# Optimization experiments

Hardware: AMD Instinct MI355X
Metric: run time of the kernel (lower is better)

Reference implementation:

```python
import jax, jax.numpy as jnp
import numpy as np

N, E, C, F = 20000, 320000, 64, 8
DIN = 2 * C + F + 1           # MLP input: sender scalars + receiver scalars + radial feats + length
AVG = 16.0                    # avg_num_neighbors
INV_SQRT3 = 0.5773502691896258


def setup_inputs() -> dict:
    key = jax.random.key(0)
    ks = jax.random.split(key, 16)
    d = {}
    d["node_feats"] = jax.random.normal(ks[0], (N, C + 3 * C), jnp.float32)  # 64x0e + 64x1o (mul-major)
    d["edge_attrs"] = jax.random.normal(ks[1], (E, 4), jnp.float32)           # SH: 1x0e + 1x1o
    d["edge_feats"] = jax.random.normal(ks[2], (E, F), jnp.float32)           # radial basis
    d["lengths"] = jax.random.uniform(ks[3], (E, 1), jnp.float32)
    d["edge_index"] = jax.random.randint(ks[4], (2, E), 0, N, jnp.int32)      # (sender, receiver)
    d["Wsc"] = jax.random.normal(ks[5], (C, C), jnp.float32) / np.sqrt(C).astype(np.float32)
    d["Wup0"] = jax.random.normal(ks[6], (C, C), jnp.float32) / np.sqrt(C).astype(np.float32)
    d["Wup1"] = jax.random.normal(ks[7], (C, C), jnp.float32) / np.sqrt(C).astype(np.float32)
    d["W1"] = jax.random.normal(ks[8], (DIN, C), jnp.float32) / np.sqrt(DIN).astype(np.float32)
    d["b1"] = jnp.zeros((C,), jnp.float32)
    d["W2"] = jax.random.normal(ks[9], (C, C), jnp.float32) / np.sqrt(C).astype(np.float32)
    d["b2"] = jnp.zeros((C,), jnp.float32)
    d["W3"] = jax.random.normal(ks[10], (C, 4 * C), jnp.float32) * 1e-3       # near-zero init like the source
    d["Ws"] = jax.random.normal(ks[11], (2 * C, C), jnp.float32) / np.sqrt(2 * C).astype(np.float32)
    d["Wv"] = jax.random.normal(ks[12], (2 * C, C), jnp.float32) / np.sqrt(2 * C).astype(np.float32)
    return d


def reference(node_feats, edge_attrs, edge_feats, lengths, edge_index,
              Wsc, Wup0, Wup1, W1, b1, W2, b2, W3, Ws, Wv):
    n = node_feats.shape[0]
    s = node_feats[:, :C]                          # [N,C] scalar (0e) channels
    v = node_feats[:, C:].reshape(n, C, 3)         # [N,C,3] vector (1o) channels

    node_scalars = s @ Wsc                          # linear_scalar -> 64x0e
    s_up = s @ Wup0                                 # linear_up, 0e block
    v_up = jnp.einsum('nci,cd->ndi', v, Wup1)       # linear_up, 1o block

    snd, rcv = edge_index[0], edge_index[1]

    # weight MLP: Dense->silu->Dense->silu->Dense(no bias)
    mlp_in = jnp.concatenate([node_scalars[snd], node_scalars[rcv], edge_feats, lengths], axis=-1)
    h = jax.nn.silu(mlp_in @ W1 + b1)
    h = jax.nn.silu(h @ W2 + b2)
    tw = h @ W3                                     # [E, 4C] per-irrep tp weights
    w0, w1, w2, w3 = jnp.split(tw, 4, axis=-1)

    y0 = edge_attrs[:, :1]                          # [E,1] SH l=0
    y1 = edge_attrs[:, 1:4]                         # [E,3] SH l=1
    xs = s_up[snd]                                  # [E,C]   gather senders
    xv = v_up[snd]                                  # [E,C,3]

    # weighted tensor product paths (component normalization), filtered to 0e/1o
    p0 = xs * y0 * w0                                               # 0e x 0e -> 0e  [E,C]
    p1 = (jnp.einsum('eci,ei->ec', xv, y1) * INV_SQRT3) * w1        # 1o x 1o -> 0e  [E,C]
    p2 = xs[:, :, None] * y1[:, None, :] * w2[:, :, None]           # 0e x 1o -> 1o  [E,C,3]
    p3 = xv * y0[:, :, None] * w3[:, :, None]                       # 1o x 0e -> 1o  [E,C,3]

    # scatter_sum messages into receiver nodes
    m0 = jax.ops.segment_sum(jnp.concatenate([p0, p1], axis=-1), rcv, num_segments=n)  # [N,2C]
    m1 = jax.ops.segment_sum(jnp.concatenate([p2, p3], axis=1), rcv, num_segments=n)   # [N,2C,3]

    # final equivariant linear on simplified irreps_mid (128x0e + 128x1o), / avg_num_neighbors
    out_s = (m0 @ Ws) / AVG                          # [N,C]
    out_v = jnp.einsum('nci,cd->ndi', m1, Wv) / AVG  # [N,C,3]

    # reshape_irreps -> [N, channels, 1 + 3]
    return jnp.concatenate([out_s[:, :, None], out_v], axis=-1)
```

## Files before the change

### kernel.cpp

```cpp
#include <hip/hip_runtime.h>

#define N_NODES 20000
#define N_EDGES 320000
#define INV_SQRT3 0.5773502691896258f

typedef unsigned short u16;
typedef unsigned int u32;
typedef __attribute__((ext_vector_type(8))) short short8;
typedef __attribute__((ext_vector_type(8))) _Float16 half8;
typedef __attribute__((ext_vector_type(2))) __fp16 fp16x2;
typedef __attribute__((ext_vector_type(4))) float f32x4;
typedef __attribute__((ext_vector_type(4))) u32 u32x4v;

static const size_t OFF_NSBF = 0;
static const size_t OFF_SV   = 2560000;
static const size_t OFF_MG   = 23040000;
static const size_t OFF_TW   = 64000000;
static const size_t OFF_W1F  = 227840000;
static const size_t OFF_W2F  = 227860480;
static const size_t OFF_W3F  = 227868672;
static const size_t OFF_WNF  = 227901440;
static const size_t OFF_CNT  = 227950592;
static const size_t OFF_OFFS = 228030592;
static const size_t OFF_CUR  = 228110608;
static const size_t OFF_SS   = 229470608;
static const size_t OFF_RS   = 230750608;
static const size_t OFF_EA   = 232030608;
static const size_t OFF_EF   = 237150608;
static const size_t OFF_LEN  = 242270608;

static __device__ __forceinline__ u16 f2bf(float x) {
    union { float f; u32 u; } c; c.f = x;
    u32 u = c.u + 0x7fffu + ((c.u >> 16) & 1u);
    return (u16)(u >> 16);
}
static __device__ __forceinline__ float bf2f(u16 b) {
    union { u32 u; float f; } c; c.u = (u32)b << 16; return c.f;
}
static __device__ __forceinline__ u16 f2h(float x) {
    union { _Float16 h; u16 u; } c; c.h = (_Float16)x; return c.u;
}
static __device__ __forceinline__ float h2f(u32 b) {
    union { u16 u; _Float16 h; } c; c.u = (u16)b; return (float)c.h;
}
static __device__ __forceinline__ u32 pkh(float a, float b) {
    union { fp16x2 h; u32 u; } c;
    c.h = __builtin_amdgcn_cvt_pkrtz(a, b);
    return c.u;
}
static __device__ __forceinline__ f32x4 mfma16(short8 a, short8 b, f32x4 c) {
    return __builtin_amdgcn_mfma_f32_16x16x32_bf16(a, b, c, 0, 0, 0);
}
static __device__ __forceinline__ f32x4 mfma16h(half8 a, half8 b, f32x4 c) {
    return __builtin_amdgcn_mfma_f32_16x16x32_f16(a, b, c, 0, 0, 0);
}
static __device__ __forceinline__ float silu(float x) {
    return x / (1.0f + __expf(-x));
}
template <typename T>
static __device__ __forceinline__ T ntload(const T* p) { return __builtin_nontemporal_load(p); }
template <typename T>
static __device__ __forceinline__ void ntstore(T* p, T v) { __builtin_nontemporal_store(v, p); }

__global__ void prep_w_kernel(const float* __restrict__ W1, const float* __restrict__ W2,
                              const float* __restrict__ W3,
                              u16* __restrict__ W1f, u16* __restrict__ W2f, u16* __restrict__ W3f) {
    int t = blockIdx.x * 256 + threadIdx.x;
    if (t >= 3840) return;
    int l = t & 63, grp = t >> 6;
    int hi = l >> 4, lo = l & 15;
    if (grp < 20) {
        int kk = grp >> 2, jt = grp & 3;
#pragma unroll
        for (int e2 = 0; e2 < 8; e2++) {
            int k = kk * 32 + hi * 8 + e2, j = jt * 16 + lo;
            W1f[(size_t)(grp * 64 + l) * 8 + e2] = (k < 137) ? f2bf(W1[k * 64 + j]) : (u16)0;
        }
    } else if (grp < 28) {
        int g = grp - 20; int kk = g >> 2, jt = g & 3;
#pragma unroll
        for (int e2 = 0; e2 < 8; e2++) {
            int k = kk * 32 + hi * 8 + e2, j = jt * 16 + lo;
            int kp = ((k & 3) << 4) + (k >> 2);
            W2f[(size_t)(g * 64 + l) * 8 + e2] = f2h(W2[kp * 64 + j]);
        }
    } else {
        int g = grp - 28; int kk = g >> 4, jt = g & 15;
#pragma unroll
        for (int e2 = 0; e2 < 8; e2++) {
            int k = kk * 32 + hi * 8 + e2, j = jt * 16 + lo;
            int kp = ((k & 3) << 4) + (k >> 2);
            W3f[(size_t)(g * 64 + l) * 8 + e2] = f2h(W3[kp * 256 + j]);
        }
    }
}

__global__ void prep_wn_kernel(const float* __restrict__ Wsc, const float* __restrict__ Wup0,
                               const float* __restrict__ Wup1, u16* __restrict__ WNF) {
    int t = blockIdx.x * 256 + threadIdx.x;
    if (t >= 1536) return;
    int mat = t >> 9;
    int rem = t & 511;
    int g = rem >> 6, l = rem & 63;
    int kk = g >> 2, jt = g & 3, hi = l >> 4, lo = l & 15;
    const float* W = (mat == 0) ? Wsc : (mat == 1) ? Wup0 : Wup1;
    u16* dh = WNF + (size_t)mat * 8192 + (size_t)(g * 64 + l) * 8;
    u16* dl = dh + 4096;
#pragma unroll
    for (int e2 = 0; e2 < 8; e2++) {
        int k = kk * 32 + hi * 8 + e2, d = jt * 16 + lo;
        float w = W[k * 64 + d];
        u16 h = f2bf(w);
        dh[e2] = h;
        dl[e2] = f2bf(w - bf2f(h));
    }
}

__global__ void prep_w2_kernel(const float* __restrict__ Ws, const float* __restrict__ Wv,
                               u16* __restrict__ WSF) {
    int t = blockIdx.x * 256 + threadIdx.x;
    if (t >= 2048) return;
    int l = t & 63, grp = t >> 6;
    int wsel = grp >> 4;
    int g = grp & 15;
    int kk = g >> 2, jt = g & 3;
    int hi = l >> 4, lo = l & 15;
    const float* W = wsel ? Wv : Ws;
    u16* dh = WSF + (size_t)wsel * 16384;
    u16* dl = dh + 8192;
    size_t base = (size_t)(g * 64 + l) * 8;
#pragma unroll
    for (int e2 = 0; e2 < 8; e2++) {
        int k = kk * 32 + hi * 8 + e2, d = jt * 16 + lo;
        float w = W[k * 64 + d];
        u16 h = f2bf(w);
        float r = w - bf2f(h);
        dh[base + e2] = h;
        dl[base + e2] = f2bf(r);
    }
}

__global__ __launch_bounds__(256) void node_prep_kernel(
    const float* __restrict__ node_feats, const u16* __restrict__ WNF,
    u16* __restrict__ ns_bf, u16* __restrict__ svh) {
    const int tid = threadIdx.x;
    const int lane = tid & 63;
    const int w = tid >> 6;
    const int lo16 = lane & 15;
    const int hi = lane >> 4;
    const int nb = blockIdx.x * 64 + w * 16;

    int an = nb + lo16; if (an > N_NODES - 1) an = N_NODES - 1;
    const float* arow = node_feats + (size_t)an * 256;

    const short8* B = (const short8*)WNF;

    f32x4 acc_ns[4], acc_su[4], acc_v[3][4];
#pragma unroll
    for (int jt = 0; jt < 4; jt++) {
        acc_ns[jt] = (f32x4)(0.0f);
        acc_su[jt] = (f32x4)(0.0f);
#pragma unroll
        for (int i = 0; i < 3; i++) acc_v[i][jt] = (f32x4)(0.0f);
    }

#pragma unroll
    for (int kk = 0; kk < 2; kk++) {
        short8 sh, sl;
        {
            const float* sp = arow + kk * 32 + hi * 8;
            f32x4 x0 = *(const f32x4*)sp;
            f32x4 x1 = *(const f32x4*)(sp + 4);
#pragma unroll
            for (int j = 0; j < 4; j++) {
                u16 h0 = f2bf(x0[j]);
                sh[j] = (short)h0;
                sl[j] = (short)f2bf(x0[j] - bf2f(h0));
                u16 h1 = f2bf(x1[j]);
                sh[4 + j] = (short)h1;
                sl[4 + j] = (short)f2bf(x1[j] - bf2f(h1));
            }
        }
        short8 vh[3], vl[3];
#pragma unroll
        for (int i = 0; i < 3; i++) {
            const float* vp = arow + 64 + i + 3 * (kk * 32 + hi * 8);
#pragma unroll
            for (int e = 0; e < 8; e++) {
                float x = vp[e * 3];
                u16 hb = f2bf(x);
                vh[i][e] = (short)hb;
                vl[i][e] = (short)f2bf(x - bf2f(hb));
            }
        }
#pragma unroll
        for (int jt = 0; jt < 4; jt++) {
            int fi = (kk * 4 + jt) * 64 + lane;
            short8 bh = B[fi], bl = B[512 + fi];
            acc_ns[jt] = mfma16(sh, bh, acc_ns[jt]);
            acc_ns[jt] = mfma16(sl, bh, acc_ns[jt]);
            acc_ns[jt] = mfma16(sh, bl, acc_ns[jt]);
            bh = B[1024 + fi]; bl = B[1536 + fi];
            acc_su[jt] = mfma16(sh, bh, acc_su[jt]);
            acc_su[jt] = mfma16(sl, bh, acc_su[jt]);
            acc_su[jt] = mfma16(sh, bl, acc_su[jt]);
            bh = B[2048 + fi]; bl = B[2560 + fi];
#pragma unroll
            for (int i = 0; i < 3; i++) {
                acc_v[i][jt] = mfma16(vh[i], bh, acc_v[i][jt]);
                acc_v[i][jt] = mfma16(vl[i], bh, acc_v[i][jt]);
                acc_v[i][jt] = mfma16(vh[i], bl, acc_v[i][jt]);
            }
        }
    }

#pragma unroll
    for (int r = 0; r < 4; r++) {
        int n = nb + hi * 4 + r;
        if (n < N_NODES) {
#pragma unroll
            for (int jt = 0; jt < 4; jt++) {
                int d = jt * 16 + lo16;
                ns_bf[(size_t)n * 64 + d] = f2bf(acc_ns[jt][r]);
                uint2 o;
                o.x = pkh(acc_su[jt][r], acc_v[0][jt][r]);
                o.y = pkh(acc_v[1][jt][r], acc_v[2][jt][r]);
                *(uint2*)&svh[((size_t)n * 64 + d) * 4] = o;
            }
        }
    }
}

__global__ void hist_kernel(const int* __restrict__ ei, int* __restrict__ cnt) {
    int e = blockIdx.x * 256 + threadIdx.x;
    if (e < N_EDGES) atomicAdd(&cnt[ei[N_EDGES + e]], 1);
}

__global__ void scan_kernel(const int* __restrict__ cnt, int* __restrict__ offs,
                            int* __restrict__ cursor) {
    __shared__ int buf[1024];
    int t = threadIdx.x;
    int base = t * 20;
    int loc[20];
    int tot = 0;
    int v20[20];
    if (base < N_NODES) {
#pragma unroll
        for (int q = 0; q < 5; q++) {
            int4 vv = *(const int4*)&cnt[base + q * 4];
            v20[q * 4 + 0] = vv.x; v20[q * 4 + 1] = vv.y;
            v20[q * 4 + 2] = vv.z; v20[q * 4 + 3] = vv.w;
        }
    } else {
#pragma unroll
        for (int i = 0; i < 20; i++) v20[i] = 0;
    }
#pragma unroll
    for (int i = 0; i < 20; i++) { loc[i] = tot; tot += v20[i]; }
    buf[t] = tot;
    __syncthreads();
    for (int d = 1; d < 1024; d <<= 1) {
        int add = (t >= d) ? buf[t - d] : 0;
        __syncthreads();
        buf[t] += add;
        __syncthreads();
    }
    int ebase = buf[t] - tot;
#pragma unroll
    for (int i = 0; i < 20; i++) {
        int idx = base + i;
        if (idx < N_NODES) { int o = ebase + loc[i]; offs[idx] = o; cursor[idx] = o; }
    }
    if (t == 1023) offs[N_NODES] = buf[1023];
}

__global__ void scatter_kernel(const int* __restrict__ ei, const float* __restrict__ edge_attrs,
                               const float* __restrict__ edge_feats, const float* __restrict__ lengths,
                               int* __restrict__ cursor,
                               int* __restrict__ ssort, int* __restrict__ rsort,
                               float* __restrict__ easort, u16* __restrict__ efsort,
                               u16* __restrict__ lsort) {
    int e = blockIdx.x * 256 + threadIdx.x;
    if (e < N_EDGES) {
        int sn = ei[e];
        int rc = ei[N_EDGES + e];
        float4 ea = *(const float4*)(edge_attrs + (size_t)e * 4);
        float4 f0 = *(const float4*)(edge_feats + (size_t)e * 8);
        float4 f1 = *(const float4*)(edge_feats + (size_t)e * 8 + 4);
        float len = lengths[e];
        uint4 pk;
        pk.x = (u32)f2bf(f0.x) | ((u32)f2bf(f0.y) << 16);
        pk.y = (u32)f2bf(f0.z) | ((u32)f2bf(f0.w) << 16);
        pk.z = (u32)f2bf(f1.x) | ((u32)f2bf(f1.y) << 16);
        pk.w = (u32)f2bf(f1.z) | ((u32)f2bf(f1.w) << 16);
        int pos = atomicAdd(&cursor[rc], 1);
        ssort[pos] = sn;
        rsort[pos] = rc;
        *(float4*)(easort + (size_t)pos * 4) = ea;
        *(uint4*)(efsort + (size_t)pos * 8) = pk;
        lsort[pos] = f2bf(len);
    }
}

__global__ __launch_bounds__(256, 5) void mlp_kernel(
    const u16* __restrict__ ns_bf,
    const u16* __restrict__ W1f, const u16* __restrict__ W2f, const u16* __restrict__ W3f,
    const float* __restrict__ b1, const float* __restrict__ b2,
    const int* __restrict__ ssort, const int* __restrict__ rsort,
    const u16* __restrict__ efsort, const u16* __restrict__ lsort,
    u16* __restrict__ twg) {

    __shared__ u16 mlpbuf[64][168];
    __shared__ u16 h1s[64][72];
    u16* h2sf = &mlpbuf[0][0];

    const int tid = threadIdx.x;
    const int l = tid & 63;
    const int lo16 = l & 15;
    const int hi = l >> 4;
    const int w = tid >> 6;
    const int erow = (w << 4) | lo16;
    const int koff = hi * 8;
    const int drow = (w << 4) + hi * 4;

    const int p0 = blockIdx.x * 64;

    const short8* w1frag = (const short8*)W1f;
    const half8* w2frag = (const half8*)W2f;
    const half8* w3frag = (const half8*)W3f;

    float bb1[4], bb2[4];
#pragma unroll
    for (int jt = 0; jt < 4; jt++) { bb1[jt] = b1[jt * 16 + lo16]; bb2[jt] = b2[jt * 16 + lo16]; }

    {
        int rr = tid >> 2, pp = tid & 3;
        uint4 z = {0, 0, 0, 0};
        *(uint4*)&mlpbuf[rr][136 + pp * 8] = z;
    }

    {
        int es = tid >> 2, part = tid & 3;
        int sn = ssort[p0 + es];
        int rc = rsort[p0 + es];
        const uint4* ps = (const uint4*)(ns_bf + (size_t)sn * 64 + part * 16);
        uint4 s0 = ps[0], s1 = ps[1];
        *(uint4*)&mlpbuf[es][part * 16] = s0;
        *(uint4*)&mlpbuf[es][part * 16 + 8] = s1;
        const uint4* pr = (const uint4*)(ns_bf + (size_t)rc * 64 + part * 16);
        uint4 r0v = pr[0], r1v = pr[1];
        *(uint4*)&mlpbuf[es][64 + part * 16] = r0v;
        *(uint4*)&mlpbuf[es][64 + part * 16 + 8] = r1v;
        if (part == 0) {
            uint4 pk = *(const uint4*)(efsort + (size_t)(p0 + es) * 8);
            *(uint4*)&mlpbuf[es][128] = pk;
            mlpbuf[es][136] = lsort[p0 + es];
        }
    }

    f32x4 a1c[4];
#pragma unroll
    for (int jt = 0; jt < 4; jt++) a1c[jt] = (f32x4)(0.0f);
    __builtin_amdgcn_s_setprio(1);
#pragma unroll
    for (int kk = 0; kk < 5; kk++) {
        short8 af = *(const short8*)&mlpbuf[erow][kk * 32 + koff];
        const short8* wb = w1frag + kk * 256 + l;
        a1c[0] = mfma16(af, wb[0],   a1c[0]);
        a1c[1] = mfma16(af, wb[64],  a1c[1]);
        a1c[2] = mfma16(af, wb[128], a1c[2]);
        a1c[3] = mfma16(af, wb[192], a1c[3]);
    }
    __builtin_amdgcn_s_setprio(0);
#pragma unroll
    for (int r = 0; r < 4; r++) {
        uint2 pk;
        pk.x = pkh(silu(a1c[0][r] + bb1[0]), silu(a1c[1][r] + bb1[1]));
        pk.y = pkh(silu(a1c[2][r] + bb1[2]), silu(a1c[3][r] + bb1[3]));
        *(uint2*)&h1s[drow + r][lo16 * 4] = pk;
    }

    f32x4 a2c[4];
#pragma unroll
    for (int jt = 0; jt < 4; jt++) a2c[jt] = (f32x4)(0.0f);
    __builtin_amdgcn_s_setprio(1);
#pragma unroll
    for (int kk = 0; kk < 2; kk++) {
        half8 af = *(const half8*)&h1s[erow][kk * 32 + koff];
        const half8* wb = w2frag + kk * 256 + l;
        a2c[0] = mfma16h(af, wb[0],   a2c[0]);
        a2c[1] = mfma16h(af, wb[64],  a2c[1]);
        a2c[2] = mfma16h(af, wb[128], a2c[2]);
        a2c[3] = mfma16h(af, wb[192], a2c[3]);
    }
    __builtin_amdgcn_s_setprio(0);
#pragma unroll
    for (int r = 0; r < 4; r++) {
        uint2 pk;
        pk.x = pkh(silu(a2c[0][r] + bb2[0]), silu(a2c[1][r] + bb2[1]));
        pk.y = pkh(silu(a2c[2][r] + bb2[2]), silu(a2c[3][r] + bb2[3]));
        *(uint2*)&h2sf[(drow + r) * 72 + lo16 * 4] = pk;
    }

    f32x4 tw[16];
#pragma unroll
    for (int jt = 0; jt < 16; jt++) tw[jt] = (f32x4)(0.0f);
    __builtin_amdgcn_s_setprio(1);
#pragma unroll
    for (int kk = 0; kk < 2; kk++) {
        half8 af = *(const half8*)&h2sf[erow * 72 + kk * 32 + koff];
        const half8* wb = w3frag + kk * 1024 + l;
#pragma unroll
        for (int jt = 0; jt < 16; jt++) tw[jt] = mfma16h(af, wb[jt * 64], tw[jt]);
    }
    __builtin_amdgcn_s_setprio(0);

    int relrow = p0 + drow;
#pragma unroll
    for (int r = 0; r < 4; r++) {
        u16* dst = twg + (size_t)(relrow + r) * 256 + lo16 * 4;
#pragma unroll
        for (int jt4 = 0; jt4 < 4; jt4++) {
            uint2 pk;
            pk.x = pkh(tw[jt4][r],     tw[4 + jt4][r]);
            pk.y = pkh(tw[8 + jt4][r], tw[12 + jt4][r]);
            *(uint2*)(dst + jt4 * 64) = pk;
        }
    }
}

__global__ __launch_bounds__(256, 4) void seg_kernel(
    const u16* __restrict__ svh, const float* __restrict__ easort,
    const int* __restrict__ ssort,
    const int* __restrict__ offs, const u16* __restrict__ twg,
    float* __restrict__ m_g) {
    const int lane = threadIdx.x & 63;
    const int wv = threadIdx.x >> 6;
    const int n = blockIdx.x * 4 + wv;
    const int c = lane;
    const int e0 = offs[n], e1 = offs[n + 1];
    float a_m0 = 0.f, a_m0b = 0.f;
    float a20 = 0.f, a21 = 0.f, a22 = 0.f, a30 = 0.f, a31 = 0.f, a32 = 0.f;
#pragma unroll 4
    for (int pos = e0; pos < e1; ++pos) {
        int sn = ssort[pos];
        uint2 tq = *(const uint2*)(twg + (size_t)pos * 256 + c * 4);
        f32x4 y4 = *(const f32x4*)(easort + (size_t)pos * 4);
        uint2 sp = *(const uint2*)&svh[((size_t)sn * 64 + c) * 4];
        float w0 = h2f(tq.x & 0xffffu);
        float w1 = h2f(tq.x >> 16);
        float w2 = h2f(tq.y & 0xffffu);
        float w3 = h2f(tq.y >> 16);
        float xs  = h2f(sp.x & 0xffffu);
        float xv0 = h2f(sp.x >> 16);
        float xv1 = h2f(sp.y & 0xffffu);
        float xv2 = h2f(sp.y >> 16);
        float y0 = y4.x, ya = y4.y, yb = y4.z, yc = y4.w;
        a_m0 = fmaf(xs * y0, w0, a_m0);
        float dv = xv0 * ya + xv1 * yb + xv2 * yc;
        a_m0b = fmaf(dv, w1, a_m0b);
        float sw2 = xs * w2;
        a20 = fmaf(sw2, ya, a20); a21 = fmaf(sw2, yb, a21); a22 = fmaf(sw2, yc, a22);
        float yw3 = y0 * w3;
        a30 = fmaf(xv0, yw3, a30); a31 = fmaf(xv1, yw3, a31); a32 = fmaf(xv2, yw3, a32);
    }
    float* mr = m_g + (size_t)n * 512;
    ntstore(mr + c,        a_m0);
    ntstore(mr + 64 + c,   a_m0b * INV_SQRT3);
    ntstore(mr + 128 + c,  a20);
    ntstore(mr + 192 + c,  a30);
    ntstore(mr + 256 + c,  a21);
    ntstore(mr + 320 + c,  a31);
    ntstore(mr + 384 + c,  a22);
    ntstore(mr + 448 + c,  a32);
}

__global__ __launch_bounds__(256, 2) void out_kernel(
    const float* __restrict__ m_g, const u16* __restrict__ WSF,
    float* __restrict__ out) {
    const int tid = threadIdx.x;
    const int lane = tid & 63;
    const int w = tid >> 6;
    const int lo16 = lane & 15;
    const int hi = lane >> 4;
    const int nb = blockIdx.x * 64 + w * 16;

    int arow_n = nb + lo16;
    if (arow_n > N_NODES - 1) arow_n = N_NODES - 1;
    const float* arow = m_g + (size_t)arow_n * 512 + hi * 8;

    const short8* bsh = (const short8*)WSF;
    const short8* bsl = (const short8*)(WSF + 8192);
    const short8* bvh = (const short8*)(WSF + 16384);
    const short8* bvl = (const short8*)(WSF + 24576);

    f32x4 acc[4][4];
#pragma unroll
    for (int q = 0; q < 4; q++)
#pragma unroll
        for (int jt = 0; jt < 4; jt++) acc[q][jt] = (f32x4)(0.0f);

#pragma unroll
    for (int kk = 0; kk < 4; kk++) {
        short8 ahi[4], alo[4];
#pragma unroll
        for (int q = 0; q < 4; q++) {
            const float* p = arow + q * 128 + kk * 32;
            f32x4 x0 = ntload((const f32x4*)p);
            f32x4 x1 = ntload((const f32x4*)(p + 4));
#pragma unroll
            for (int j = 0; j < 4; j++) {
                u16 h0 = f2bf(x0[j]);
                ahi[q][j] = (short)h0;
                alo[q][j] = (short)f2bf(x0[j] - bf2f(h0));
                u16 h1 = f2bf(x1[j]);
                ahi[q][4 + j] = (short)h1;
                alo[q][4 + j] = (short)f2bf(x1[j] - bf2f(h1));
            }
        }
#pragma unroll
        for (int jt = 0; jt < 4; jt++) {
            int bidx = (kk * 4 + jt) * 64 + lane;
            short8 wh_s = bsh[bidx];
            short8 wl_s = bsl[bidx];
            short8 wh_v = bvh[bidx];
            short8 wl_v = bvl[bidx];
            acc[0][jt] = mfma16(ahi[0], wh_s, acc[0][jt]);
            acc[0][jt] = mfma16(alo[0], wh_s, acc[0][jt]);
            acc[0][jt] = mfma16(ahi[0], wl_s, acc[0][jt]);
#pragma unroll
            for (int q = 1; q < 4; q++) {
                acc[q][jt] = mfma16(ahi[q], wh_v, acc[q][jt]);
                acc[q][jt] = mfma16(alo[q], wh_v, acc[q][jt]);
                acc[q][jt] = mfma16(ahi[q], wl_v, acc[q][jt]);
            }
        }
    }

#pragma unroll
    for (int r = 0; r < 4; r++) {
        int n = nb + hi * 4 + r;
        if (n < N_NODES) {
#pragma unroll
            for (int jt = 0; jt < 4; jt++) {
                int d = jt * 16 + lo16;
                f32x4 o;
                o.x = acc[0][jt][r] * 0.0625f;
                o.y = acc[1][jt][r] * 0.0625f;
                o.z = acc[2][jt][r] * 0.0625f;
                o.w = acc[3][jt][r] * 0.0625f;
                ntstore((f32x4*)(out + (size_t)n * 256 + d * 4), o);
            }
        }
    }
}

extern "C" void kernel_launch(void* const* d_in, const int* in_sizes, int n_in,
                              void* d_out, int out_size, void* d_ws, size_t ws_size,
                              hipStream_t stream) {
    (void)in_sizes; (void)n_in; (void)out_size; (void)ws_size;
    const float* node_feats = (const float*)d_in[0];
    const float* edge_attrs = (const float*)d_in[1];
    const float* edge_feats = (const float*)d_in[2];
    const float* lengths    = (const float*)d_in[3];
    const int*   edge_index = (const int*)d_in[4];
    const float* Wsc  = (const float*)d_in[5];
    const float* Wup0 = (const float*)d_in[6];
    const float* Wup1 = (const float*)d_in[7];
    const float* W1   = (const float*)d_in[8];
    const float* b1   = (const float*)d_in[9];
    const float* W2   = (const float*)d_in[10];
    const float* b2   = (const float*)d_in[11];
    const float* W3   = (const float*)d_in[12];
    const float* Ws   = (const float*)d_in[13];
    const float* Wv   = (const float*)d_in[14];

    char* ws = (char*)d_ws;
    u16*   ns_bf  = (u16*)(ws + OFF_NSBF);
    u16*   svh    = (u16*)(ws + OFF_SV);
    float* m_g    = (float*)(ws + OFF_MG);
    u16*   twg    = (u16*)(ws + OFF_TW);
    u16*   W1f    = (u16*)(ws + OFF_W1F);
    u16*   W2f    = (u16*)(ws + OFF_W2F);
    u16*   W3f    = (u16*)(ws + OFF_W3F);
    u16*   WNF    = (u16*)(ws + OFF_WNF);
    int*   cnt    = (int*)(ws + OFF_CNT);
    int*   offs   = (int*)(ws + OFF_OFFS);
    int*   cursor = (int*)(ws + OFF_CUR);
    u16*   WSF    = (u16*)(ws + OFF_CUR);
    int*   ssort  = (int*)(ws + OFF_SS);
    int*   rsort  = (int*)(ws + OFF_RS);
    float* easort = (float*)(ws + OFF_EA);
    u16*   efsort = (u16*)(ws + OFF_EF);
    u16*   lsort  = (u16*)(ws + OFF_LEN);
    float* out    = (float*)d_out;

    (void)hipMemsetAsync(cnt, 0, N_NODES * sizeof(int), stream);
    prep_w_kernel<<<15, 256, 0, stream>>>(W1, W2, W3, W1f, W2f, W3f);
    prep_wn_kernel<<<6, 256, 0, stream>>>(Wsc, Wup0, Wup1, WNF);
    node_prep_kernel<<<(N_NODES + 63) / 64, 256, 0, stream>>>(node_feats, WNF, ns_bf, svh);
    hist_kernel<<<N_EDGES / 256, 256, 0, stream>>>(edge_index, cnt);
    scan_kernel<<<1, 1024, 0, stream>>>(cnt, offs, cursor);
    scatter_kernel<<<N_EDGES / 256, 256, 0, stream>>>(edge_index, edge_attrs, edge_feats,
                                                      lengths, cursor,
                                                      ssort, rsort, easort, efsort, lsort);
    prep_w2_kernel<<<8, 256, 0, stream>>>(Ws, Wv, WSF);

    mlp_kernel<<<N_EDGES / 64, 256, 0, stream>>>(ns_bf, W1f, W2f, W3f, b1, b2,
                                                 ssort, rsort, efsort, lsort, twg);
    seg_kernel<<<N_NODES / 4, 256, 0, stream>>>(svh, easort, ssort,
                                                offs, twg, m_g);
    out_kernel<<<(N_NODES + 63) / 64, 256, 0, stream>>>(m_g, WSF, out);
}
```

Baseline: 233.0 us.

## Load MLP input fragments directly from global into registers, skipping LDS staging

The MLP kernel no longer stages sender/receiver scalars and edge features in a 64x168 shared buffer. Each lane now loads its MFMA A-fragments straight from global memory into registers. To make that possible, the scatter kernel writes a padded 32-element per-edge record holding the radial features, the length and zero padding, so the fifth K-chunk is a single aligned load. Shared memory per block drops, and launch bounds go from 5 to 6 blocks per SM for higher occupancy. In exchange, global gather loads are less coalesced (16-byte per-lane reads), the per-edge write in scatter grows to 64 bytes, and register pressure may rise under the tighter launch bound.

```diff
diff --git a/kernel.cpp b/kernel.cpp
--- a/kernel.cpp
+++ b/kernel.cpp
@@ -26,8 +26,7 @@
 static const size_t OFF_SS   = 229470608;
 static const size_t OFF_RS   = 230750608;
 static const size_t OFF_EA   = 232030608;
-static const size_t OFF_EF   = 237150608;
-static const size_t OFF_LEN  = 242270608;
+static const size_t OFF_ED   = 237150608;
 
 static __device__ __forceinline__ u16 f2bf(float x) {
     union { float f; u32 u; } c; c.f = x;
@@ -278,8 +277,7 @@
                                const float* __restrict__ edge_feats, const float* __restrict__ lengths,
                                int* __restrict__ cursor,
                                int* __restrict__ ssort, int* __restrict__ rsort,
-                               float* __restrict__ easort, u16* __restrict__ efsort,
-                               u16* __restrict__ lsort) {
+                               float* __restrict__ easort, u16* __restrict__ edata) {
     int e = blockIdx.x * 256 + threadIdx.x;
     if (e < N_EDGES) {
         int sn = ei[e];
@@ -297,22 +295,26 @@
         ssort[pos] = sn;
         rsort[pos] = rc;
         *(float4*)(easort + (size_t)pos * 4) = ea;
-        *(uint4*)(efsort + (size_t)pos * 8) = pk;
-        lsort[pos] = f2bf(len);
-    }
-}
-
-__global__ __launch_bounds__(256, 5) void mlp_kernel(
+        u16* ed = edata + (size_t)pos * 32;
+        *(uint4*)ed = pk;
+        uint4 t1 = {(u32)f2bf(len), 0, 0, 0};
+        *(uint4*)(ed + 8) = t1;
+        uint4 z = {0, 0, 0, 0};
+        *(uint4*)(ed + 16) = z;
+        *(uint4*)(ed + 24) = z;
+    }
+}
+
+__global__ __launch_bounds__(256, 6) void mlp_kernel(
     const u16* __restrict__ ns_bf,
     const u16* __restrict__ W1f, const u16* __restrict__ W2f, const u16* __restrict__ W3f,
     const float* __restrict__ b1, const float* __restrict__ b2,
     const int* __restrict__ ssort, const int* __restrict__ rsort,
-    const u16* __restrict__ efsort, const u16* __restrict__ lsort,
+    const u16* __restrict__ edata,
     u16* __restrict__ twg) {
 
-    __shared__ u16 mlpbuf[64][168];
     __shared__ u16 h1s[64][72];
-    u16* h2sf = &mlpbuf[0][0];
+    __shared__ u16 h2s[64][72];
 
     const int tid = threadIdx.x;
     const int l = tid & 63;
@@ -324,6 +326,7 @@
     const int drow = (w << 4) + hi * 4;
 
     const int p0 = blockIdx.x * 64;
+    const int eidx = p0 + erow;
 
     const short8* w1frag = (const short8*)W1f;
     const half8* w2frag = (const half8*)W2f;
@@ -333,43 +336,43 @@
 #pragma unroll
     for (int jt = 0; jt < 4; jt++) { bb1[jt] = b1[jt * 16 + lo16]; bb2[jt] = b2[jt * 16 + lo16]; }
 
-    {
-        int rr = tid >> 2, pp = tid & 3;
-        uint4 z = {0, 0, 0, 0};
-        *(uint4*)&mlpbuf[rr][136 + pp * 8] = z;
-    }
-
-    {
-        int es = tid >> 2, part = tid & 3;
-        int sn = ssort[p0 + es];
-        int rc = rsort[p0 + es];
-        const uint4* ps = (const uint4*)(ns_bf + (size_t)sn * 64 + part * 16);
-        uint4 s0 = ps[0], s1 = ps[1];
-        *(uint4*)&mlpbuf[es][part * 16] = s0;
-        *(uint4*)&mlpbuf[es][part * 16 + 8] = s1;
-        const uint4* pr = (const uint4*)(ns_bf + (size_t)rc * 64 + part * 16);
-        uint4 r0v = pr[0], r1v = pr[1];
-        *(uint4*)&mlpbuf[es][64 + part * 16] = r0v;
-        *(uint4*)&mlpbuf[es][64 + part * 16 + 8] = r1v;
-        if (part == 0) {
-            uint4 pk = *(const uint4*)(efsort + (size_t)(p0 + es) * 8);
-            *(uint4*)&mlpbuf[es][128] = pk;
-            mlpbuf[es][136] = lsort[p0 + es];
-        }
-    }
+    int sn = ssort[eidx];
+    int rc = rsort[eidx];
+    const u16* sbase = ns_bf + (size_t)sn * 64 + koff;
+    const u16* rbase = ns_bf + (size_t)rc * 64 + koff;
+    const u16* ebase = edata + (size_t)eidx * 32 + koff;
+    short8 a0 = *(const short8*)sbase;
+    short8 a1 = *(const short8*)(sbase + 32);
+    short8 a2 = *(const short8*)rbase;
+    short8 a3 = *(const short8*)(rbase + 32);
+    short8 a4 = *(const short8*)ebase;
 
     f32x4 a1c[4];
 #pragma unroll
     for (int jt = 0; jt < 4; jt++) a1c[jt] = (f32x4)(0.0f);
     __builtin_amdgcn_s_setprio(1);
-#pragma unroll
-    for (int kk = 0; kk < 5; kk++) {
-        short8 af = *(const short8*)&mlpbuf[erow][kk * 32 + koff];
-        const short8* wb = w1frag + kk * 256 + l;
-        a1c[0] = mfma16(af, wb[0],   a1c[0]);
-        a1c[1] = mfma16(af, wb[64],  a1c[1]);
-        a1c[2] = mfma16(af, wb[128], a1c[2]);
-        a1c[3] = mfma16(af, wb[192], a1c[3]);
+    {
+        const short8* wb = w1frag + l;
+        a1c[0] = mfma16(a0, wb[0],          a1c[0]);
+        a1c[1] = mfma16(a0, wb[64],         a1c[1]);
+        a1c[2] = mfma16(a0, wb[128],        a1c[2]);
+        a1c[3] = mfma16(a0, wb[192],        a1c[3]);
+        a1c[0] = mfma16(a1, wb[256],        a1c[0]);
+        a1c[1] = mfma16(a1, wb[320],        a1c[1]);
+        a1c[2] = mfma16(a1, wb[384],        a1c[2]);
+        a1c[3] = mfma16(a1, wb[448],        a1c[3]);
+        a1c[0] = mfma16(a2, wb[512],        a1c[0]);
+        a1c[1] = mfma16(a2, wb[576],        a1c[1]);
+        a1c[2] = mfma16(a2, wb[640],        a1c[2]);
+        a1c[3] = mfma16(a2, wb[704],        a1c[3]);
+        a1c[0] = mfma16(a3, wb[768],        a1c[0]);
+        a1c[1] = mfma16(a3, wb[832],        a1c[1]);
+        a1c[2] = mfma16(a3, wb[896],        a1c[2]);
+        a1c[3] = mfma16(a3, wb[960],        a1c[3]);
+        a1c[0] = mfma16(a4, wb[1024],       a1c[0]);
+        a1c[1] = mfma16(a4, wb[1088],       a1c[1]);
+        a1c[2] = mfma16(a4, wb[1152],       a1c[2]);
+        a1c[3] = mfma16(a4, wb[1216],       a1c[3]);
     }
     __builtin_amdgcn_s_setprio(0);
 #pragma unroll
@@ -399,7 +402,7 @@
         uint2 pk;
         pk.x = pkh(silu(a2c[0][r] + bb2[0]), silu(a2c[1][r] + bb2[1]));
         pk.y = pkh(silu(a2c[2][r] + bb2[2]), silu(a2c[3][r] + bb2[3]));
-        *(uint2*)&h2sf[(drow + r) * 72 + lo16 * 4] = pk;
+        *(uint2*)&h2s[drow + r][lo16 * 4] = pk;
     }
 
     f32x4 tw[16];
@@ -408,7 +411,7 @@
     __builtin_amdgcn_s_setprio(1);
 #pragma unroll
     for (int kk = 0; kk < 2; kk++) {
-        half8 af = *(const half8*)&h2sf[erow * 72 + kk * 32 + koff];
+        half8 af = *(const half8*)&h2s[erow][kk * 32 + koff];
         const half8* wb = w3frag + kk * 1024 + l;
 #pragma unroll
         for (int jt = 0; jt < 16; jt++) tw[jt] = mfma16h(af, wb[jt * 64], tw[jt]);
@@ -591,8 +594,7 @@
     int*   ssort  = (int*)(ws + OFF_SS);
     int*   rsort  = (int*)(ws + OFF_RS);
     float* easort = (float*)(ws + OFF_EA);
-    u16*   efsort = (u16*)(ws + OFF_EF);
-    u16*   lsort  = (u16*)(ws + OFF_LEN);
+    u16*   edata  = (u16*)(ws + OFF_ED);
     float* out    = (float*)d_out;
 
     (void)hipMemsetAsync(cnt, 0, N_NODES * sizeof(int), stream);
@@ -603,11 +605,11 @@
     scan_kernel<<<1, 1024, 0, stream>>>(cnt, offs, cursor);
     scatter_kernel<<<N_EDGES / 256, 256, 0, stream>>>(edge_index, edge_attrs, edge_feats,
                                                       lengths, cursor,
-                                                      ssort, rsort, easort, efsort, lsort);
+                                                      ssort, rsort, easort, edata);
     prep_w2_kernel<<<8, 256, 0, stream>>>(Ws, Wv, WSF);
 
     mlp_kernel<<<N_EDGES / 64, 256, 0, stream>>>(ns_bf, W1f, W2f, W3f, b1, b2,
-                                                 ssort, rsort, efsort, lsort, twg);
+                                                 ssort, rsort, edata, twg);
     seg_kernel<<<N_NODES / 4, 256, 0, stream>>>(svh, easort, ssort,
                                                 offs, twg, m_g);
     out_kernel<<<(N_NODES + 63) / 64, 256, 0, stream>>>(m_g, WSF, out);
```

Measured after the change: 261.8 us. 1.12x slower.
